# Performance work log

Hardware: AMD Instinct MI355X
Metric: run time of the kernel (lower is better)

The kernel has to match this reference:

```python
import jax, jax.numpy as jnp
import numpy as np

H_IMG, W_IMG = 48, 64  # feature-map resolution hard-coded in the module
NUM_HEADS = 8


def get_positional_encodings(B, N, dtype=jnp.float32):
    # (p3^2, p4^2, p3*p4, p3, p4, 1) on normalized grid; intrinsics=None path
    ys = jnp.linspace(-1.0, 1.0, H_IMG, dtype=dtype)
    xs = jnp.linspace(-1.0, 1.0, W_IMG, dtype=dtype)
    p3 = jnp.tile(ys, W_IMG)           # [N] = ys repeated W times (torch repeat)
    p4 = jnp.repeat(xs, H_IMG)         # [N] = each x repeated H times
    pos = jnp.stack([p3 * p3, p4 * p4, p3 * p4, p3, p4, jnp.ones_like(p3)], axis=-1)  # [N,6]
    return jnp.broadcast_to(pos[None], (B, N, 6))


def setup_inputs() -> dict:
    key = jax.random.key(0)
    k1, k2, k3, k4, k5 = jax.random.split(key, 5)
    B, N, C = 2, H_IMG * W_IMG, 256
    s = 0.02
    return {
        "x1": jax.random.normal(k1, (B, N, C), jnp.float32),
        "x2": jax.random.normal(k2, (B, N, C), jnp.float32),
        "Wq": jax.random.normal(k3, (C, C), jnp.float32) * s,      # qkv (one-way: q only)
        "Wkv": jax.random.normal(k4, (C, 2 * C), jnp.float32) * s,  # qkv2 -> k,v
        "Wpf": jax.random.normal(k5, (C + 6 * NUM_HEADS, C), jnp.float32) * s,  # proj_fundamental
        "bpf": jnp.zeros((C,), jnp.float32),
    }


def reference(x1, x2, Wq, Wkv, Wpf, bpf):
    B, N, C = x1.shape
    H = NUM_HEADS
    d = C // H
    scale = d ** -0.5

    # q from x1; k,v from x2 (separate linear, matching torch reshape/permute split)
    q1 = (x1 @ Wq).reshape(B, N, H, d).transpose(0, 2, 1, 3)          # [B,H,N,d]
    kv = (x2 @ Wkv).reshape(B, N, 2, H, d)
    k2 = kv[:, :, 0].transpose(0, 2, 1, 3)                            # [B,H,N,d]
    v2 = kv[:, :, 1].transpose(0, 2, 1, 3)                            # [B,H,N,d]

    attn = jax.nn.softmax(jnp.einsum('bhnd,bhmd->bhnm', q1, k2) * scale, axis=-1)  # [B,H,N,N]

    pos = get_positional_encodings(B, N, x1.dtype)                    # [B,N,6]
    v2p = jnp.concatenate(
        [v2, jnp.broadcast_to(pos[:, None], (B, H, N, 6))], axis=-1)  # [B,H,N,d+6]

    y = jnp.einsum('bhnm,bhmd->bhnd', attn, v2p)                      # [B,H,N,d+6]
    y = y.transpose(0, 2, 1, 3).reshape(B, N, H * (d + 6))            # [B,N,C+6H]
    y = y @ Wpf + bpf                                                 # [B,N,C]
    y = y.reshape(B, N, H, d).transpose(0, 2, 1, 3)                   # [B,H,N,d]

    return jnp.concatenate([attn, y], axis=-1)                        # [B,H,N,N+d]
```

## Files before the change

kernel.cpp:

```cpp
#include <hip/hip_runtime.h>
#include <hip/hip_bf16.h>
#include <cstdint>
#include <cstddef>

#define NB 2
#define NH 8
#define BHN 16
#define NN 3072
#define CC 256
#define DD 32
#define OUTW 3104
#define VW 48
#define KP 384

typedef __attribute__((ext_vector_type(8))) __bf16 bf16x8;
typedef __attribute__((ext_vector_type(4))) short short4v;
typedef __attribute__((ext_vector_type(4))) float f32x4;

static __device__ __forceinline__ unsigned short f2bf(float f) {
    __hip_bfloat16 h = __float2bfloat16(f);
    return *reinterpret_cast<unsigned short*>(&h);
}

static __device__ __forceinline__ bf16x8 ldb8(const unsigned short* p) {
    return *(const bf16x8*)p;
}

static __device__ __forceinline__ f32x4 mfma16(bf16x8 a, bf16x8 b, f32x4 c) {
    return __builtin_amdgcn_mfma_f32_16x16x32_bf16(a, b, c, 0, 0, 0);
}

static __device__ __forceinline__ float bfhi2f(unsigned u) {
    union { unsigned u; float f; } v; v.u = u & 0xffff0000u; return v.f;
}
static __device__ __forceinline__ float bflo2f(unsigned u) {
    union { unsigned u; float f; } v; v.u = u << 16; return v.f;
}

__global__ __launch_bounds__(256) void prep_kernel(
    const float* __restrict__ x1, const float* __restrict__ x2,
    const float* __restrict__ Wq, const float* __restrict__ Wkv,
    const float* __restrict__ Wpf,
    unsigned short* __restrict__ x1b, unsigned short* __restrict__ x2b,
    unsigned short* __restrict__ Wt, unsigned short* __restrict__ Wpft,
    unsigned short* __restrict__ v2pT)
{
    int i = blockIdx.x * 256 + threadIdx.x;
    const int S_X = NB * NN * CC;
    if (i < S_X) { x1b[i] = f2bf(x1[i]); return; }
    i -= S_X;
    if (i < S_X) { x2b[i] = f2bf(x2[i]); return; }
    i -= S_X;
    const int S_WT = 768 * CC;
    if (i < S_WT) {
        int j = i >> 8, kk = i & 255;
        float w = (j < 256) ? Wq[kk * 256 + j] : Wkv[kk * 512 + (j - 256)];
        Wt[i] = f2bf(w);
        return;
    }
    i -= S_WT;
    const int S_WP = 256 * KP;
    if (i < S_WP) {
        int c2 = i / KP, t = i - c2 * KP;
        int h = t / VW, cc = t - h * VW;
        unsigned short v = 0;
        if (cc < 38) v = f2bf(Wpf[(h * 38 + cc) * 256 + c2]);
        Wpft[i] = v;
        return;
    }
    i -= S_WP;
    const int S_POS = BHN * 16 * NN;
    if (i < S_POS) {
        int n = i % NN;
        int r = i / NN;
        int bh = r >> 4;
        int c = (r & 15) + 32;
        float val = 0.f;
        if (c < 38) {
            float p3 = -1.f + 2.f * (float)(n % 48) / 47.f;
            float p4 = -1.f + 2.f * (float)(n / 48) / 63.f;
            float pv[6] = { p3 * p3, p4 * p4, p3 * p4, p3, p4, 1.f };
            val = pv[c - 32];
        }
        v2pT[((size_t)bh * VW + c) * NN + n] = f2bf(val);
    }
}

__global__ __launch_bounds__(256) void qkv_kernel(
    const unsigned short* __restrict__ x1b, const unsigned short* __restrict__ x2b,
    const unsigned short* __restrict__ Wt,
    unsigned short* __restrict__ qbh, unsigned short* __restrict__ kbh,
    unsigned short* __restrict__ v2pT)
{
    int rt = blockIdx.x, ct = blockIdx.y;
    int wv = threadIdx.x >> 6, lane = threadIdx.x & 63;
    int g = lane >> 4, q = lane & 15;
    int row0 = rt * 64 + wv * 16;
    const unsigned short* A = (ct < 4) ? x1b : x2b;
    const unsigned short* arow = A + (size_t)(row0 + q) * CC + g * 8;
    const unsigned short* brow = Wt + (size_t)(ct * 64 + q) * CC + g * 8;
    f32x4 acc[4];
    #pragma unroll
    for (int cb = 0; cb < 4; ++cb) acc[cb] = f32x4{0.f, 0.f, 0.f, 0.f};
    for (int k0 = 0; k0 < CC; k0 += 32) {
        bf16x8 af = ldb8(arow + k0);
        #pragma unroll
        for (int cb = 0; cb < 4; ++cb)
            acc[cb] = mfma16(af, ldb8(brow + (size_t)cb * 16 * CC + k0), acc[cb]);
    }
    int b = row0 / NN, nb = row0 % NN;
    #pragma unroll
    for (int cb = 0; cb < 4; ++cb) {
        int jj = ct * 64 + cb * 16 + q;
        #pragma unroll
        for (int r = 0; r < 4; ++r) {
            int n = nb + 4 * g + r;
            unsigned short bv = f2bf(acc[cb][r]);
            if (jj < 256) {
                int h = jj >> 5, c = jj & 31;
                qbh[(size_t)((b * NH + h) * NN + n) * DD + c] = bv;
            } else if (jj < 512) {
                int jk = jj - 256; int h = jk >> 5, c = jk & 31;
                kbh[(size_t)((b * NH + h) * NN + n) * DD + c] = bv;
            } else {
                int jv = jj - 512; int h = jv >> 5, c = jv & 31;
                v2pT[(size_t)((b * NH + h) * VW + c) * NN + n] = bv;
            }
        }
    }
}

__global__ __launch_bounds__(256) void attn_kernel(
    const unsigned short* __restrict__ qbh, const unsigned short* __restrict__ kbh,
    const unsigned short* __restrict__ v2pT,
    float* __restrict__ out, unsigned short* __restrict__ yacc)
{
    __shared__ unsigned short ptile[4][16][256];
    const float C = 0.17677669529663687f * 1.4426950408889634f;

    int id = blockIdx.x;
    int xcd = id & 7;
    int slot = id >> 3;
    int bh = xcd * 2 + (slot & 1);
    int qt = slot >> 1;

    int wv = threadIdx.x >> 6, lane = threadIdx.x & 63;
    int g = lane >> 4, q = lane & 15;
    int qrow = qt * 64 + wv * 16;

    bf16x8 qf = ldb8(qbh + (size_t)(bh * NN + qrow + q) * DD + g * 8);
    const unsigned short* kbase = kbh + (size_t)bh * NN * DD;
    const unsigned short* vbase = v2pT + (size_t)bh * VW * NN;

    float l = 0.f;
    {
        bf16x8 kf0 = ldb8(kbase + (size_t)(q) * DD + g * 8);
        bf16x8 kf1 = ldb8(kbase + (size_t)(16 + q) * DD + g * 8);
        for (int it = 0; it < 96; ++it) {
            int m0 = it * 32;
            bf16x8 kn0 = ldb8(kbase + (size_t)(m0 + 32 + q) * DD + g * 8);
            bf16x8 kn1 = ldb8(kbase + (size_t)(m0 + 48 + q) * DD + g * 8);
            f32x4 z = {0.f, 0.f, 0.f, 0.f};
            f32x4 s0 = mfma16(kf0, qf, z);
            f32x4 s1 = mfma16(kf1, qf, z);
            #pragma unroll
            for (int r = 0; r < 4; ++r)
                l += exp2f(s0[r] * C) + exp2f(s1[r] * C);
            kf0 = kn0; kf1 = kn1;
        }
    }
    l += __shfl_xor(l, 16, 64);
    l += __shfl_xor(l, 32, 64);
    float nl2 = -__log2f(l);

    f32x4 yt0 = {0.f,0.f,0.f,0.f}, yt1 = yt0, yt2 = yt0;
    char* myt = (char*)&ptile[wv][0][0];
    char* prow = myt + q * 512;
    unsigned swq = (unsigned)((q & 7) << 4);

    bf16x8 kf0 = ldb8(kbase + (size_t)(q) * DD + g * 8);
    bf16x8 kf1 = ldb8(kbase + (size_t)(16 + q) * DD + g * 8);
    bf16x8 vf0 = ldb8(vbase + (size_t)(q) * NN + g * 8);
    bf16x8 vf1 = ldb8(vbase + (size_t)(16 + q) * NN + g * 8);
    bf16x8 vf2 = ldb8(vbase + (size_t)(32 + q) * NN + g * 8);

    for (int ph = 0; ph < 12; ++ph) {
        #pragma unroll
        for (int it2 = 0; it2 < 8; ++it2) {
            int m0 = ph * 256 + it2 * 32;
            bf16x8 kn0 = ldb8(kbase + (size_t)(m0 + 32 + q) * DD + g * 8);
            bf16x8 kn1 = ldb8(kbase + (size_t)(m0 + 48 + q) * DD + g * 8);
            bf16x8 vn0 = ldb8(vbase + (size_t)(q) * NN + m0 + 32 + g * 8);
            bf16x8 vn1 = ldb8(vbase + (size_t)(16 + q) * NN + m0 + 32 + g * 8);
            bf16x8 vn2 = ldb8(vbase + (size_t)(32 + q) * NN + m0 + 32 + g * 8);

            f32x4 z = {0.f, 0.f, 0.f, 0.f};
            f32x4 s0 = mfma16(kf0, qf, z);
            f32x4 s1 = mfma16(kf1, qf, z);
            short4v pk0, pk1;
            #pragma unroll
            for (int r = 0; r < 4; ++r) {
                pk0[r] = (short)f2bf(exp2f(__builtin_fmaf(s0[r], C, nl2)));
                pk1[r] = (short)f2bf(exp2f(__builtin_fmaf(s1[r], C, nl2)));
            }
            unsigned b0 = (unsigned)(it2 * 64 + 8 * g);
            *(short4v*)(prow + (b0 ^ swq)) = pk0;
            *(short4v*)(prow + ((b0 + 32) ^ swq)) = pk1;
            asm volatile("s_waitcnt lgkmcnt(0)" ::: "memory");
            __builtin_amdgcn_sched_barrier(0);
            bf16x8 pf = *(const bf16x8*)(prow + ((unsigned)(it2 * 64 + 16 * g) ^ swq));
            yt0 = mfma16(vf0, pf, yt0);
            yt1 = mfma16(vf1, pf, yt1);
            yt2 = mfma16(vf2, pf, yt2);
            kf0 = kn0; kf1 = kn1; vf0 = vn0; vf1 = vn1; vf2 = vn2;
        }
        #pragma unroll
        for (int i = 0; i < 16; ++i) {
            unsigned off = ((unsigned)(lane * 8)) ^ ((unsigned)((i & 7) << 4));
            uint2 d = *(const uint2*)(myt + i * 512 + off);
            f32x4 v;
            v[0] = bflo2f(d.x); v[1] = bfhi2f(d.x);
            v[2] = bflo2f(d.y); v[3] = bfhi2f(d.y);
            float* dst = out + (size_t)(bh * NN + qrow + i) * OUTW + ph * 256 + lane * 4;
            __builtin_nontemporal_store(v, (f32x4*)dst);
        }
    }

    int b = bh >> 3, h = bh & 7;
    int nrow = qrow + q;
    unsigned short* yrow = yacc + (size_t)(b * NN + nrow) * KP + h * VW;
    f32x4 yts[3] = { yt0, yt1, yt2 };
    #pragma unroll
    for (int cb = 0; cb < 3; ++cb) {
        short4v pk;
        #pragma unroll
        for (int r = 0; r < 4; ++r) pk[r] = (short)f2bf(yts[cb][r]);
        *(short4v*)(yrow + cb * 16 + 4 * g) = pk;
    }
}

__global__ __launch_bounds__(256) void proj_kernel(
    const unsigned short* __restrict__ yacc, const unsigned short* __restrict__ Wpft,
    const float* __restrict__ bpf, float* __restrict__ out)
{
    int rt = blockIdx.x, ct = blockIdx.y;
    int wv = threadIdx.x >> 6, lane = threadIdx.x & 63;
    int g = lane >> 4, q = lane & 15;
    int row0 = rt * 64 + wv * 16;
    const unsigned short* arow = yacc + (size_t)(row0 + q) * KP + g * 8;
    const unsigned short* b0 = Wpft + (size_t)(ct * 64 + q) * KP + g * 8;
    f32x4 acc[4];
    #pragma unroll
    for (int cb = 0; cb < 4; ++cb) acc[cb] = f32x4{0.f, 0.f, 0.f, 0.f};
    for (int k0 = 0; k0 < KP; k0 += 32) {
        bf16x8 af = ldb8(arow + k0);
        #pragma unroll
        for (int cb = 0; cb < 4; ++cb)
            acc[cb] = mfma16(af, ldb8(b0 + (size_t)cb * 16 * KP + k0), acc[cb]);
    }
    int b = row0 / NN, nb = row0 % NN;
    #pragma unroll
    for (int cb = 0; cb < 4; ++cb) {
        int c2 = ct * 64 + cb * 16 + q;
        float bias = bpf[c2];
        int h = c2 >> 5, c = c2 & 31;
        float* obase = out + (size_t)((b * NH + h) * NN) * OUTW + NN + c;
        #pragma unroll
        for (int r = 0; r < 4; ++r) {
            int n = nb + 4 * g + r;
            __builtin_nontemporal_store(acc[cb][r] + bias, &obase[(size_t)n * OUTW]);
        }
    }
}

extern "C" void kernel_launch(void* const* d_in, const int* in_sizes, int n_in,
                              void* d_out, int out_size, void* d_ws, size_t ws_size,
                              hipStream_t stream)
{
    (void)in_sizes; (void)n_in; (void)out_size; (void)ws_size;
    const float* x1  = (const float*)d_in[0];
    const float* x2  = (const float*)d_in[1];
    const float* Wq  = (const float*)d_in[2];
    const float* Wkv = (const float*)d_in[3];
    const float* Wpf = (const float*)d_in[4];
    const float* bpf = (const float*)d_in[5];
    float* out = (float*)d_out;
    char* ws = (char*)d_ws;

    unsigned short* x1b  = (unsigned short*)(ws + 0);
    unsigned short* x2b  = (unsigned short*)(ws + 3145728);
    unsigned short* Wt   = (unsigned short*)(ws + 6291456);
    unsigned short* Wpft = (unsigned short*)(ws + 6684672);
    unsigned short* qbh  = (unsigned short*)(ws + 6881280);
    unsigned short* kbh  = (unsigned short*)(ws + 10027008);
    unsigned short* v2pT = (unsigned short*)(ws + 13172736);
    unsigned short* yacc = (unsigned short*)(ws + 17891328);

    prep_kernel<<<16512, 256, 0, stream>>>(x1, x2, Wq, Wkv, Wpf, x1b, x2b, Wt, Wpft, v2pT);
    qkv_kernel<<<dim3(96, 12), 256, 0, stream>>>(x1b, x2b, Wt, qbh, kbh, v2pT);
    attn_kernel<<<768, 256, 0, stream>>>(qbh, kbh, v2pT, out, yacc);
    proj_kernel<<<dim3(96, 4), 256, 0, stream>>>(yacc, Wpft, bpf, out);
}
```

Baseline: 240.7 us.

## Specialize attention waves: two compute P tiles, one streams them to output

Splits each attention block into two compute waves that write softmax probability tiles into a double-buffered shared-memory area, and a third wave that converts and stores the previous phase's tile to the output. The aim is to overlap the large attention-matrix global stores with the QK/PV MFMA work instead of interleaving them in each wave. Blocks now cover 32 query rows and the grid doubles. The per-phase barriers tie compute progress to the single store wave's throughput, so the store wave could become the bottleneck.

```diff
diff --git a/kernel.cpp b/kernel.cpp
--- a/kernel.cpp
+++ b/kernel.cpp
@@ -130,12 +130,12 @@
     }
 }
 
-__global__ __launch_bounds__(256) void attn_kernel(
+__global__ __launch_bounds__(192) void attn_kernel(
     const unsigned short* __restrict__ qbh, const unsigned short* __restrict__ kbh,
     const unsigned short* __restrict__ v2pT,
     float* __restrict__ out, unsigned short* __restrict__ yacc)
 {
-    __shared__ unsigned short ptile[4][16][256];
+    __shared__ unsigned short buf[2][32][256];
     const float C = 0.17677669529663687f * 1.4426950408889634f;
 
     int id = blockIdx.x;
@@ -143,99 +143,125 @@
     int slot = id >> 3;
     int bh = xcd * 2 + (slot & 1);
     int qt = slot >> 1;
+    int qrow0 = qt * 32;
 
     int wv = threadIdx.x >> 6, lane = threadIdx.x & 63;
     int g = lane >> 4, q = lane & 15;
-    int qrow = qt * 64 + wv * 16;
-
-    bf16x8 qf = ldb8(qbh + (size_t)(bh * NN + qrow + q) * DD + g * 8);
+
     const unsigned short* kbase = kbh + (size_t)bh * NN * DD;
     const unsigned short* vbase = v2pT + (size_t)bh * VW * NN;
 
-    float l = 0.f;
-    {
+    if (wv < 2) {
+        int qrow = qrow0 + wv * 16;
+        bf16x8 qf = ldb8(qbh + (size_t)(bh * NN + qrow + q) * DD + g * 8);
+
+        float l = 0.f;
+        {
+            bf16x8 kf0 = ldb8(kbase + (size_t)(q) * DD + g * 8);
+            bf16x8 kf1 = ldb8(kbase + (size_t)(16 + q) * DD + g * 8);
+            for (int it = 0; it < 96; ++it) {
+                int m0 = it * 32;
+                bf16x8 kn0 = ldb8(kbase + (size_t)(m0 + 32 + q) * DD + g * 8);
+                bf16x8 kn1 = ldb8(kbase + (size_t)(m0 + 48 + q) * DD + g * 8);
+                f32x4 z = {0.f, 0.f, 0.f, 0.f};
+                f32x4 s0 = mfma16(kf0, qf, z);
+                f32x4 s1 = mfma16(kf1, qf, z);
+                #pragma unroll
+                for (int r = 0; r < 4; ++r)
+                    l += exp2f(s0[r] * C) + exp2f(s1[r] * C);
+                kf0 = kn0; kf1 = kn1;
+            }
+        }
+        l += __shfl_xor(l, 16, 64);
+        l += __shfl_xor(l, 32, 64);
+        float nl2 = -__log2f(l);
+
+        f32x4 yt0 = {0.f,0.f,0.f,0.f}, yt1 = yt0, yt2 = yt0;
+        unsigned swq = (unsigned)((q & 7) << 4);
+
         bf16x8 kf0 = ldb8(kbase + (size_t)(q) * DD + g * 8);
         bf16x8 kf1 = ldb8(kbase + (size_t)(16 + q) * DD + g * 8);
-        for (int it = 0; it < 96; ++it) {
-            int m0 = it * 32;
-            bf16x8 kn0 = ldb8(kbase + (size_t)(m0 + 32 + q) * DD + g * 8);
-            bf16x8 kn1 = ldb8(kbase + (size_t)(m0 + 48 + q) * DD + g * 8);
-            f32x4 z = {0.f, 0.f, 0.f, 0.f};
-            f32x4 s0 = mfma16(kf0, qf, z);
-            f32x4 s1 = mfma16(kf1, qf, z);
+        bf16x8 vf0 = ldb8(vbase + (size_t)(q) * NN + g * 8);
+        bf16x8 vf1 = ldb8(vbase + (size_t)(16 + q) * NN + g * 8);
+        bf16x8 vf2 = ldb8(vbase + (size_t)(32 + q) * NN + g * 8);
+
+        for (int ph = 0; ph < 12; ++ph) {
+            char* prow = (char*)&buf[ph & 1][wv * 16 + q][0];
             #pragma unroll
-            for (int r = 0; r < 4; ++r)
-                l += exp2f(s0[r] * C) + exp2f(s1[r] * C);
-            kf0 = kn0; kf1 = kn1;
-        }
-    }
-    l += __shfl_xor(l, 16, 64);
-    l += __shfl_xor(l, 32, 64);
-    float nl2 = -__log2f(l);
-
-    f32x4 yt0 = {0.f,0.f,0.f,0.f}, yt1 = yt0, yt2 = yt0;
-    char* myt = (char*)&ptile[wv][0][0];
-    char* prow = myt + q * 512;
-    unsigned swq = (unsigned)((q & 7) << 4);
-
-    bf16x8 kf0 = ldb8(kbase + (size_t)(q) * DD + g * 8);
-    bf16x8 kf1 = ldb8(kbase + (size_t)(16 + q) * DD + g * 8);
-    bf16x8 vf0 = ldb8(vbase + (size_t)(q) * NN + g * 8);
-    bf16x8 vf1 = ldb8(vbase + (size_t)(16 + q) * NN + g * 8);
-    bf16x8 vf2 = ldb8(vbase + (size_t)(32 + q) * NN + g * 8);
-
-    for (int ph = 0; ph < 12; ++ph) {
-        #pragma unroll
-        for (int it2 = 0; it2 < 8; ++it2) {
-            int m0 = ph * 256 + it2 * 32;
-            bf16x8 kn0 = ldb8(kbase + (size_t)(m0 + 32 + q) * DD + g * 8);
-            bf16x8 kn1 = ldb8(kbase + (size_t)(m0 + 48 + q) * DD + g * 8);
-            bf16x8 vn0 = ldb8(vbase + (size_t)(q) * NN + m0 + 32 + g * 8);
-            bf16x8 vn1 = ldb8(vbase + (size_t)(16 + q) * NN + m0 + 32 + g * 8);
-            bf16x8 vn2 = ldb8(vbase + (size_t)(32 + q) * NN + m0 + 32 + g * 8);
-
-            f32x4 z = {0.f, 0.f, 0.f, 0.f};
-            f32x4 s0 = mfma16(kf0, qf, z);
-            f32x4 s1 = mfma16(kf1, qf, z);
-            short4v pk0, pk1;
+            for (int it2 = 0; it2 < 8; ++it2) {
+                int m0 = ph * 256 + it2 * 32;
+                bf16x8 kn0 = ldb8(kbase + (size_t)(m0 + 32 + q) * DD + g * 8);
+                bf16x8 kn1 = ldb8(kbase + (size_t)(m0 + 48 + q) * DD + g * 8);
+                bf16x8 vn0 = ldb8(vbase + (size_t)(q) * NN + m0 + 32 + g * 8);
+                bf16x8 vn1 = ldb8(vbase + (size_t)(16 + q) * NN + m0 + 32 + g * 8);
+                bf16x8 vn2 = ldb8(vbase + (size_t)(32 + q) * NN + m0 + 32 + g * 8);
+
+                f32x4 z = {0.f, 0.f, 0.f, 0.f};
+                f32x4 s0 = mfma16(kf0, qf, z);
+                f32x4 s1 = mfma16(kf1, qf, z);
+                short4v pk0, pk1;
+                #pragma unroll
+                for (int r = 0; r < 4; ++r) {
+                    pk0[r] = (short)f2bf(exp2f(__builtin_fmaf(s0[r], C, nl2)));
+                    pk1[r] = (short)f2bf(exp2f(__builtin_fmaf(s1[r], C, nl2)));
+                }
+                unsigned b0 = (unsigned)(it2 * 64 + 8 * g);
+                *(short4v*)(prow + (b0 ^ swq)) = pk0;
+                *(short4v*)(prow + ((b0 + 32) ^ swq)) = pk1;
+                asm volatile("s_waitcnt lgkmcnt(0)" ::: "memory");
+                __builtin_amdgcn_sched_barrier(0);
+                bf16x8 pf = *(const bf16x8*)(prow + ((unsigned)(it2 * 64 + 16 * g) ^ swq));
+                yt0 = mfma16(vf0, pf, yt0);
+                yt1 = mfma16(vf1, pf, yt1);
+                yt2 = mfma16(vf2, pf, yt2);
+                kf0 = kn0; kf1 = kn1; vf0 = vn0; vf1 = vn1; vf2 = vn2;
+            }
+            __syncthreads();
+        }
+
+        int b = bh >> 3, h = bh & 7;
+        unsigned short* yrow = yacc + (size_t)(b * NN + qrow + q) * KP + h * VW;
+        f32x4 yts[3] = { yt0, yt1, yt2 };
+        #pragma unroll
+        for (int cb = 0; cb < 3; ++cb) {
+            short4v pk;
             #pragma unroll
-            for (int r = 0; r < 4; ++r) {
-                pk0[r] = (short)f2bf(exp2f(__builtin_fmaf(s0[r], C, nl2)));
-                pk1[r] = (short)f2bf(exp2f(__builtin_fmaf(s1[r], C, nl2)));
-            }
-            unsigned b0 = (unsigned)(it2 * 64 + 8 * g);
-            *(short4v*)(prow + (b0 ^ swq)) = pk0;
-            *(short4v*)(prow + ((b0 + 32) ^ swq)) = pk1;
-            asm volatile("s_waitcnt lgkmcnt(0)" ::: "memory");
-            __builtin_amdgcn_sched_barrier(0);
-            bf16x8 pf = *(const bf16x8*)(prow + ((unsigned)(it2 * 64 + 16 * g) ^ swq));
-            yt0 = mfma16(vf0, pf, yt0);
-            yt1 = mfma16(vf1, pf, yt1);
-            yt2 = mfma16(vf2, pf, yt2);
-            kf0 = kn0; kf1 = kn1; vf0 = vn0; vf1 = vn1; vf2 = vn2;
-        }
-        #pragma unroll
-        for (int i = 0; i < 16; ++i) {
-            unsigned off = ((unsigned)(lane * 8)) ^ ((unsigned)((i & 7) << 4));
-            uint2 d = *(const uint2*)(myt + i * 512 + off);
-            f32x4 v;
-            v[0] = bflo2f(d.x); v[1] = bfhi2f(d.x);
-            v[2] = bflo2f(d.y); v[3] = bfhi2f(d.y);
-            float* dst = out + (size_t)(bh * NN + qrow + i) * OUTW + ph * 256 + lane * 4;
-            __builtin_nontemporal_store(v, (f32x4*)dst);
-        }
-    }
-
-    int b = bh >> 3, h = bh & 7;
-    int nrow = qrow + q;
-    unsigned short* yrow = yacc + (size_t)(b * NN + nrow) * KP + h * VW;
-    f32x4 yts[3] = { yt0, yt1, yt2 };
-    #pragma unroll
-    for (int cb = 0; cb < 3; ++cb) {
-        short4v pk;
-        #pragma unroll
-        for (int r = 0; r < 4; ++r) pk[r] = (short)f2bf(yts[cb][r]);
-        *(short4v*)(yrow + cb * 16 + 4 * g) = pk;
+            for (int r = 0; r < 4; ++r) pk[r] = (short)f2bf(yts[cb][r]);
+            *(short4v*)(yrow + cb * 16 + 4 * g) = pk;
+        }
+    } else {
+        for (int ph = 0; ph < 12; ++ph) {
+            if (ph > 0) {
+                int sp = ph - 1;
+                const char* src = (const char*)&buf[sp & 1][0][0];
+                float* dst0 = out + (size_t)(bh * NN + qrow0) * OUTW + sp * 256 + lane * 4;
+                #pragma unroll 8
+                for (int i = 0; i < 32; ++i) {
+                    unsigned off = ((unsigned)(lane * 8)) ^ ((unsigned)((i & 7) << 4));
+                    unsigned long long d = *(const unsigned long long*)(src + i * 512 + off);
+                    unsigned dlo = (unsigned)d, dhi = (unsigned)(d >> 32);
+                    f32x4 v;
+                    v[0] = bflo2f(dlo); v[1] = bfhi2f(dlo);
+                    v[2] = bflo2f(dhi); v[3] = bfhi2f(dhi);
+                    __builtin_nontemporal_store(v, (f32x4*)(dst0 + (size_t)i * OUTW));
+                }
+            }
+            __syncthreads();
+        }
+        {
+            const char* src = (const char*)&buf[1][0][0];
+            float* dst0 = out + (size_t)(bh * NN + qrow0) * OUTW + 11 * 256 + lane * 4;
+            #pragma unroll 8
+            for (int i = 0; i < 32; ++i) {
+                unsigned off = ((unsigned)(lane * 8)) ^ ((unsigned)((i & 7) << 4));
+                unsigned long long d = *(const unsigned long long*)(src + i * 512 + off);
+                unsigned dlo = (unsigned)d, dhi = (unsigned)(d >> 32);
+                f32x4 v;
+                v[0] = bflo2f(dlo); v[1] = bfhi2f(dlo);
+                v[2] = bflo2f(dhi); v[3] = bfhi2f(dhi);
+                __builtin_nontemporal_store(v, (f32x4*)(dst0 + (size_t)i * OUTW));
+            }
+        }
     }
 }
 
@@ -298,6 +324,6 @@
 
     prep_kernel<<<16512, 256, 0, stream>>>(x1, x2, Wq, Wkv, Wpf, x1b, x2b, Wt, Wpft, v2pT);
     qkv_kernel<<<dim3(96, 12), 256, 0, stream>>>(x1b, x2b, Wt, qbh, kbh, v2pT);
-    attn_kernel<<<768, 256, 0, stream>>>(qbh, kbh, v2pT, out, yacc);
+    attn_kernel<<<1536, 192, 0, stream>>>(qbh, kbh, v2pT, out, yacc);
     proj_kernel<<<dim3(96, 4), 256, 0, stream>>>(yacc, Wpft, bpf, out);
 }
```

Measured after the change: 256.1 us. +6.4%, slower.

## Process two query tiles per wave, overlapping next tile's row-sum pass with current output pass

Applied to the files above, without the earlier changes.

Each wave now handles 32 query rows in two 16-row tiles instead of one, and the grid is halved. The separate softmax-denominator pass for the second tile is folded into the first tile's probability/PV pass, reusing the same K fragment loads. This removes one standalone QK^T+exp sweep over K per two tiles. The cost is more serial work per block, fewer blocks for latency hiding and higher register pressure.

```diff
diff --git a/kernel.cpp b/kernel.cpp
--- a/kernel.cpp
+++ b/kernel.cpp
@@ -142,17 +142,22 @@
     int xcd = id & 7;
     int slot = id >> 3;
     int bh = xcd * 2 + (slot & 1);
-    int qt = slot >> 1;
+    int sup = slot >> 1;
 
     int wv = threadIdx.x >> 6, lane = threadIdx.x & 63;
     int g = lane >> 4, q = lane & 15;
-    int qrow = qt * 64 + wv * 16;
-
-    bf16x8 qf = ldb8(qbh + (size_t)(bh * NN + qrow + q) * DD + g * 8);
+    int qrow0 = sup * 128 + wv * 32;
+
+    bf16x8 qf0 = ldb8(qbh + (size_t)(bh * NN + qrow0 + q) * DD + g * 8);
+    bf16x8 qf1 = ldb8(qbh + (size_t)(bh * NN + qrow0 + 16 + q) * DD + g * 8);
     const unsigned short* kbase = kbh + (size_t)bh * NN * DD;
     const unsigned short* vbase = v2pT + (size_t)bh * VW * NN;
 
-    float l = 0.f;
+    char* myt = (char*)&ptile[wv][0][0];
+    char* prow = myt + q * 512;
+    unsigned swq = (unsigned)((q & 7) << 4);
+
+    float l0 = 0.f;
     {
         bf16x8 kf0 = ldb8(kbase + (size_t)(q) * DD + g * 8);
         bf16x8 kf1 = ldb8(kbase + (size_t)(16 + q) * DD + g * 8);
@@ -161,81 +166,150 @@
             bf16x8 kn0 = ldb8(kbase + (size_t)(m0 + 32 + q) * DD + g * 8);
             bf16x8 kn1 = ldb8(kbase + (size_t)(m0 + 48 + q) * DD + g * 8);
             f32x4 z = {0.f, 0.f, 0.f, 0.f};
-            f32x4 s0 = mfma16(kf0, qf, z);
-            f32x4 s1 = mfma16(kf1, qf, z);
+            f32x4 s0 = mfma16(kf0, qf0, z);
+            f32x4 s1 = mfma16(kf1, qf0, z);
             #pragma unroll
             for (int r = 0; r < 4; ++r)
-                l += exp2f(s0[r] * C) + exp2f(s1[r] * C);
+                l0 += exp2f(s0[r] * C) + exp2f(s1[r] * C);
             kf0 = kn0; kf1 = kn1;
         }
     }
-    l += __shfl_xor(l, 16, 64);
-    l += __shfl_xor(l, 32, 64);
-    float nl2 = -__log2f(l);
-
+    l0 += __shfl_xor(l0, 16, 64);
+    l0 += __shfl_xor(l0, 32, 64);
+    float nl2_0 = -__log2f(l0);
+
+    float l1 = 0.f;
     f32x4 yt0 = {0.f,0.f,0.f,0.f}, yt1 = yt0, yt2 = yt0;
-    char* myt = (char*)&ptile[wv][0][0];
-    char* prow = myt + q * 512;
-    unsigned swq = (unsigned)((q & 7) << 4);
-
-    bf16x8 kf0 = ldb8(kbase + (size_t)(q) * DD + g * 8);
-    bf16x8 kf1 = ldb8(kbase + (size_t)(16 + q) * DD + g * 8);
-    bf16x8 vf0 = ldb8(vbase + (size_t)(q) * NN + g * 8);
-    bf16x8 vf1 = ldb8(vbase + (size_t)(16 + q) * NN + g * 8);
-    bf16x8 vf2 = ldb8(vbase + (size_t)(32 + q) * NN + g * 8);
-
-    for (int ph = 0; ph < 12; ++ph) {
-        #pragma unroll
-        for (int it2 = 0; it2 < 8; ++it2) {
-            int m0 = ph * 256 + it2 * 32;
-            bf16x8 kn0 = ldb8(kbase + (size_t)(m0 + 32 + q) * DD + g * 8);
-            bf16x8 kn1 = ldb8(kbase + (size_t)(m0 + 48 + q) * DD + g * 8);
-            bf16x8 vn0 = ldb8(vbase + (size_t)(q) * NN + m0 + 32 + g * 8);
-            bf16x8 vn1 = ldb8(vbase + (size_t)(16 + q) * NN + m0 + 32 + g * 8);
-            bf16x8 vn2 = ldb8(vbase + (size_t)(32 + q) * NN + m0 + 32 + g * 8);
-
-            f32x4 z = {0.f, 0.f, 0.f, 0.f};
-            f32x4 s0 = mfma16(kf0, qf, z);
-            f32x4 s1 = mfma16(kf1, qf, z);
-            short4v pk0, pk1;
-            #pragma unroll
-            for (int r = 0; r < 4; ++r) {
-                pk0[r] = (short)f2bf(exp2f(__builtin_fmaf(s0[r], C, nl2)));
-                pk1[r] = (short)f2bf(exp2f(__builtin_fmaf(s1[r], C, nl2)));
-            }
-            unsigned b0 = (unsigned)(it2 * 64 + 8 * g);
-            *(short4v*)(prow + (b0 ^ swq)) = pk0;
-            *(short4v*)(prow + ((b0 + 32) ^ swq)) = pk1;
-            asm volatile("s_waitcnt lgkmcnt(0)" ::: "memory");
-            __builtin_amdgcn_sched_barrier(0);
-            bf16x8 pf = *(const bf16x8*)(prow + ((unsigned)(it2 * 64 + 16 * g) ^ swq));
-            yt0 = mfma16(vf0, pf, yt0);
-            yt1 = mfma16(vf1, pf, yt1);
-            yt2 = mfma16(vf2, pf, yt2);
-            kf0 = kn0; kf1 = kn1; vf0 = vn0; vf1 = vn1; vf2 = vn2;
-        }
-        #pragma unroll
-        for (int i = 0; i < 16; ++i) {
-            unsigned off = ((unsigned)(lane * 8)) ^ ((unsigned)((i & 7) << 4));
-            uint2 d = *(const uint2*)(myt + i * 512 + off);
-            f32x4 v;
-            v[0] = bflo2f(d.x); v[1] = bfhi2f(d.x);
-            v[2] = bflo2f(d.y); v[3] = bfhi2f(d.y);
-            float* dst = out + (size_t)(bh * NN + qrow + i) * OUTW + ph * 256 + lane * 4;
-            __builtin_nontemporal_store(v, (f32x4*)dst);
-        }
-    }
-
-    int b = bh >> 3, h = bh & 7;
-    int nrow = qrow + q;
-    unsigned short* yrow = yacc + (size_t)(b * NN + nrow) * KP + h * VW;
-    f32x4 yts[3] = { yt0, yt1, yt2 };
-    #pragma unroll
-    for (int cb = 0; cb < 3; ++cb) {
-        short4v pk;
-        #pragma unroll
-        for (int r = 0; r < 4; ++r) pk[r] = (short)f2bf(yts[cb][r]);
-        *(short4v*)(yrow + cb * 16 + 4 * g) = pk;
+    {
+        bf16x8 kf0 = ldb8(kbase + (size_t)(q) * DD + g * 8);
+        bf16x8 kf1 = ldb8(kbase + (size_t)(16 + q) * DD + g * 8);
+        bf16x8 vf0 = ldb8(vbase + (size_t)(q) * NN + g * 8);
+        bf16x8 vf1 = ldb8(vbase + (size_t)(16 + q) * NN + g * 8);
+        bf16x8 vf2 = ldb8(vbase + (size_t)(32 + q) * NN + g * 8);
+        for (int ph = 0; ph < 12; ++ph) {
+            #pragma unroll
+            for (int it2 = 0; it2 < 8; ++it2) {
+                int m0 = ph * 256 + it2 * 32;
+                bf16x8 kn0 = ldb8(kbase + (size_t)(m0 + 32 + q) * DD + g * 8);
+                bf16x8 kn1 = ldb8(kbase + (size_t)(m0 + 48 + q) * DD + g * 8);
+                bf16x8 vn0 = ldb8(vbase + (size_t)(q) * NN + m0 + 32 + g * 8);
+                bf16x8 vn1 = ldb8(vbase + (size_t)(16 + q) * NN + m0 + 32 + g * 8);
+                bf16x8 vn2 = ldb8(vbase + (size_t)(32 + q) * NN + m0 + 32 + g * 8);
+
+                f32x4 z = {0.f, 0.f, 0.f, 0.f};
+                f32x4 s0 = mfma16(kf0, qf0, z);
+                f32x4 s1 = mfma16(kf1, qf0, z);
+                f32x4 t0 = mfma16(kf0, qf1, z);
+                f32x4 t1 = mfma16(kf1, qf1, z);
+                short4v pk0, pk1;
+                #pragma unroll
+                for (int r = 0; r < 4; ++r) {
+                    pk0[r] = (short)f2bf(exp2f(__builtin_fmaf(s0[r], C, nl2_0)));
+                    pk1[r] = (short)f2bf(exp2f(__builtin_fmaf(s1[r], C, nl2_0)));
+                }
+                unsigned b0 = (unsigned)(it2 * 64 + 8 * g);
+                *(short4v*)(prow + (b0 ^ swq)) = pk0;
+                *(short4v*)(prow + ((b0 + 32) ^ swq)) = pk1;
+                asm volatile("s_waitcnt lgkmcnt(0)" ::: "memory");
+                __builtin_amdgcn_sched_barrier(0);
+                bf16x8 pf = *(const bf16x8*)(prow + ((unsigned)(it2 * 64 + 16 * g) ^ swq));
+                yt0 = mfma16(vf0, pf, yt0);
+                yt1 = mfma16(vf1, pf, yt1);
+                yt2 = mfma16(vf2, pf, yt2);
+                #pragma unroll
+                for (int r = 0; r < 4; ++r)
+                    l1 += exp2f(t0[r] * C) + exp2f(t1[r] * C);
+                kf0 = kn0; kf1 = kn1; vf0 = vn0; vf1 = vn1; vf2 = vn2;
+            }
+            #pragma unroll
+            for (int i = 0; i < 16; ++i) {
+                unsigned off = ((unsigned)(lane * 8)) ^ ((unsigned)((i & 7) << 4));
+                uint2 d = *(const uint2*)(myt + i * 512 + off);
+                f32x4 v;
+                v[0] = bflo2f(d.x); v[1] = bfhi2f(d.x);
+                v[2] = bflo2f(d.y); v[3] = bfhi2f(d.y);
+                float* dst = out + (size_t)(bh * NN + qrow0 + i) * OUTW + ph * 256 + lane * 4;
+                __builtin_nontemporal_store(v, (f32x4*)dst);
+            }
+        }
+    }
+    l1 += __shfl_xor(l1, 16, 64);
+    l1 += __shfl_xor(l1, 32, 64);
+    float nl2_1 = -__log2f(l1);
+
+    {
+        int b = bh >> 3, h = bh & 7;
+        unsigned short* yrow = yacc + (size_t)(b * NN + qrow0 + q) * KP + h * VW;
+        f32x4 yts[3] = { yt0, yt1, yt2 };
+        #pragma unroll
+        for (int cb = 0; cb < 3; ++cb) {
+            short4v pk;
+            #pragma unroll
+            for (int r = 0; r < 4; ++r) pk[r] = (short)f2bf(yts[cb][r]);
+            *(short4v*)(yrow + cb * 16 + 4 * g) = pk;
+        }
+    }
+
+    yt0 = f32x4{0.f,0.f,0.f,0.f}; yt1 = yt0; yt2 = yt0;
+    {
+        bf16x8 kf0 = ldb8(kbase + (size_t)(q) * DD + g * 8);
+        bf16x8 kf1 = ldb8(kbase + (size_t)(16 + q) * DD + g * 8);
+        bf16x8 vf0 = ldb8(vbase + (size_t)(q) * NN + g * 8);
+        bf16x8 vf1 = ldb8(vbase + (size_t)(16 + q) * NN + g * 8);
+        bf16x8 vf2 = ldb8(vbase + (size_t)(32 + q) * NN + g * 8);
+        for (int ph = 0; ph < 12; ++ph) {
+            #pragma unroll
+            for (int it2 = 0; it2 < 8; ++it2) {
+                int m0 = ph * 256 + it2 * 32;
+                bf16x8 kn0 = ldb8(kbase + (size_t)(m0 + 32 + q) * DD + g * 8);
+                bf16x8 kn1 = ldb8(kbase + (size_t)(m0 + 48 + q) * DD + g * 8);
+                bf16x8 vn0 = ldb8(vbase + (size_t)(q) * NN + m0 + 32 + g * 8);
+                bf16x8 vn1 = ldb8(vbase + (size_t)(16 + q) * NN + m0 + 32 + g * 8);
+                bf16x8 vn2 = ldb8(vbase + (size_t)(32 + q) * NN + m0 + 32 + g * 8);
+
+                f32x4 z = {0.f, 0.f, 0.f, 0.f};
+                f32x4 s0 = mfma16(kf0, qf1, z);
+                f32x4 s1 = mfma16(kf1, qf1, z);
+                short4v pk0, pk1;
+                #pragma unroll
+                for (int r = 0; r < 4; ++r) {
+                    pk0[r] = (short)f2bf(exp2f(__builtin_fmaf(s0[r], C, nl2_1)));
+                    pk1[r] = (short)f2bf(exp2f(__builtin_fmaf(s1[r], C, nl2_1)));
+                }
+                unsigned b0 = (unsigned)(it2 * 64 + 8 * g);
+                *(short4v*)(prow + (b0 ^ swq)) = pk0;
+                *(short4v*)(prow + ((b0 + 32) ^ swq)) = pk1;
+                asm volatile("s_waitcnt lgkmcnt(0)" ::: "memory");
+                __builtin_amdgcn_sched_barrier(0);
+                bf16x8 pf = *(const bf16x8*)(prow + ((unsigned)(it2 * 64 + 16 * g) ^ swq));
+                yt0 = mfma16(vf0, pf, yt0);
+                yt1 = mfma16(vf1, pf, yt1);
+                yt2 = mfma16(vf2, pf, yt2);
+                kf0 = kn0; kf1 = kn1; vf0 = vn0; vf1 = vn1; vf2 = vn2;
+            }
+            #pragma unroll
+            for (int i = 0; i < 16; ++i) {
+                unsigned off = ((unsigned)(lane * 8)) ^ ((unsigned)((i & 7) << 4));
+                uint2 d = *(const uint2*)(myt + i * 512 + off);
+                f32x4 v;
+                v[0] = bflo2f(d.x); v[1] = bfhi2f(d.x);
+                v[2] = bflo2f(d.y); v[3] = bfhi2f(d.y);
+                float* dst = out + (size_t)(bh * NN + qrow0 + 16 + i) * OUTW + ph * 256 + lane * 4;
+                __builtin_nontemporal_store(v, (f32x4*)dst);
+            }
+        }
+    }
+    {
+        int b = bh >> 3, h = bh & 7;
+        unsigned short* yrow = yacc + (size_t)(b * NN + qrow0 + 16 + q) * KP + h * VW;
+        f32x4 yts[3] = { yt0, yt1, yt2 };
+        #pragma unroll
+        for (int cb = 0; cb < 3; ++cb) {
+            short4v pk;
+            #pragma unroll
+            for (int r = 0; r < 4; ++r) pk[r] = (short)f2bf(yts[cb][r]);
+            *(short4v*)(yrow + cb * 16 + 4 * g) = pk;
+        }
     }
 }
 
@@ -298,6 +372,6 @@
 
     prep_kernel<<<16512, 256, 0, stream>>>(x1, x2, Wq, Wkv, Wpf, x1b, x2b, Wt, Wpft, v2pT);
     qkv_kernel<<<dim3(96, 12), 256, 0, stream>>>(x1b, x2b, Wt, qbh, kbh, v2pT);
-    attn_kernel<<<768, 256, 0, stream>>>(qbh, kbh, v2pT, out, yacc);
+    attn_kernel<<<384, 256, 0, stream>>>(qbh, kbh, v2pT, out, yacc);
     proj_kernel<<<dim3(96, 4), 256, 0, stream>>>(yacc, Wpft, bpf, out);
 }
```

New measurement: 279.1 us. +16.0%, slower.
